# Kernel tuning notes

Hardware: AMD Instinct MI355X
Metric: run time of the kernel (lower is better)

Reference implementation:

```python
import jax, jax.numpy as jnp
import numpy as np
from jax import lax

B = 128; LEADS = 12; T = 1000; DM = 128; DI = 256; DS = 16; DR = 8; DC = 4; NB = 4; L = 199; OUT = 256


def _ln(x, g, b):
    m = x.mean(-1, keepdims=True)
    v = ((x - m) ** 2).mean(-1, keepdims=True)
    return (x - m) * lax.rsqrt(v + 1e-5) * g + b


def _ssm_scan(u, delta, A, Bm, Cm, D):
    """Selective scan. u, delta: [B,L,DI]; Bm, Cm: [B,L,DS]; A: [DI,DS]; D: [DI]."""
    def step(h, inp):
        d_t, B_t, C_t, u_t = inp  # [B,DI],[B,DS],[B,DS],[B,DI]
        dA = jnp.exp(d_t[:, :, None] * A[None])            # [B,DI,DS]
        h = dA * h + (d_t * u_t)[:, :, None] * B_t[:, None, :]
        y = jnp.einsum('bds,bs->bd', h, C_t)
        return h, y
    h0 = jnp.zeros((u.shape[0], A.shape[0], A.shape[1]), u.dtype)
    xs = (jnp.moveaxis(delta, 1, 0), jnp.moveaxis(Bm, 1, 0),
          jnp.moveaxis(Cm, 1, 0), jnp.moveaxis(u, 1, 0))
    _, ys = lax.scan(step, h0, xs)
    return jnp.moveaxis(ys, 0, 1) + u * D[None, None, :]


def setup_inputs() -> dict:
    key = jax.random.key(0)
    ks = jax.random.split(key, 16)
    n = lambda k, shp, s: jax.random.normal(k, shp, jnp.float32) * s
    inp = {}
    inp['x'] = jax.random.normal(ks[0], (B, LEADS, T), jnp.float32)
    inp['pe_w'] = n(ks[1], (DM, LEADS, 10), 0.1)
    inp['pe_b'] = jnp.zeros((DM,), jnp.float32)
    inp['gn_g'] = jnp.ones((DM,), jnp.float32)
    inp['gn_b'] = jnp.zeros((DM,), jnp.float32)
    inp['pos'] = n(ks[2], (1, L, DM), 0.02)
    inp['ln1_g'] = jnp.ones((NB, DM), jnp.float32)
    inp['ln1_b'] = jnp.zeros((NB, DM), jnp.float32)
    inp['in_w'] = n(ks[3], (NB, 2 * DI, DM), 0.05)
    inp['conv_w'] = n(ks[4], (NB, DI, DC), 0.2)
    inp['conv_b'] = jnp.zeros((NB, DI), jnp.float32)
    inp['xproj_w'] = n(ks[5], (NB, DR + 2 * DS, DI), 0.05)
    inp['dtproj_w'] = n(ks[6], (NB, DI, DR), 0.2)
    inp['dtproj_b'] = jnp.full((NB, DI), -4.6, jnp.float32)  # softplus(-4.6) ~= 0.01
    inp['A_log'] = jnp.tile(jnp.log(jnp.arange(1, DS + 1, dtype=jnp.float32))[None, None, :], (NB, DI, 1))
    inp['Dp'] = jnp.ones((NB, DI), jnp.float32)
    inp['outw'] = n(ks[7], (NB, DM, DI), 0.05)
    inp['ln2_g'] = jnp.ones((NB, DM), jnp.float32)
    inp['ln2_b'] = jnp.zeros((NB, DM), jnp.float32)
    inp['ffn_w1'] = n(ks[8], (NB, 4 * DM, DM), 0.05)
    inp['ffn_b1'] = jnp.zeros((NB, 4 * DM), jnp.float32)
    inp['ffn_w2'] = n(ks[9], (NB, DM, 4 * DM), 0.05)
    inp['ffn_b2'] = jnp.zeros((NB, DM), jnp.float32)
    inp['lnf_g'] = jnp.ones((DM,), jnp.float32)
    inp['lnf_b'] = jnp.zeros((DM,), jnp.float32)
    inp['head_w'] = n(ks[10], (OUT, DM), 0.05)
    inp['head_b'] = jnp.zeros((OUT,), jnp.float32)
    return inp


def reference(x, pe_w, pe_b, gn_g, gn_b, pos, ln1_g, ln1_b, in_w, conv_w, conv_b,
              xproj_w, dtproj_w, dtproj_b, A_log, Dp, outw, ln2_g, ln2_b,
              ffn_w1, ffn_b1, ffn_w2, ffn_b2, lnf_g, lnf_b, head_w, head_b):
    # --- patch embed: Conv1d(12 -> DM, k=10, s=5) + GroupNorm(8) + GELU ---
    h = lax.conv_general_dilated(x, pe_w, (5,), 'VALID',
                                 dimension_numbers=('NCH', 'OIH', 'NCH'))
    h = h + pe_b[None, :, None]                      # [B, DM, L]
    Bb, _, Lc = h.shape
    hg = h.reshape(Bb, 8, DM // 8, Lc)
    m = hg.mean((2, 3), keepdims=True)
    v = ((hg - m) ** 2).mean((2, 3), keepdims=True)
    h = ((hg - m) * lax.rsqrt(v + 1e-5)).reshape(Bb, DM, Lc)
    h = h * gn_g[None, :, None] + gn_b[None, :, None]
    h = jax.nn.gelu(h, approximate=False)
    h = jnp.swapaxes(h, 1, 2) + pos                  # [B, L, DM]

    for i in range(NB):
        # --- Mamba block ---
        u = _ln(h, ln1_g[i], ln1_b[i])
        xz = u @ in_w[i].T                           # [B, L, 2*DI]
        xm, z = jnp.split(xz, 2, axis=-1)
        xc = jnp.swapaxes(xm, 1, 2)                  # [B, DI, L]
        xc = jnp.pad(xc, ((0, 0), (0, 0), (DC - 1, 0)))  # causal pad
        xc = lax.conv_general_dilated(xc, conv_w[i][:, None, :], (1,), 'VALID',
                                      dimension_numbers=('NCH', 'OIH', 'NCH'),
                                      feature_group_count=DI)
        xc = xc + conv_b[i][None, :, None]
        u_ssm = jax.nn.silu(jnp.swapaxes(xc, 1, 2))  # [B, L, DI]
        dbl = u_ssm @ xproj_w[i].T                   # [B, L, DR+2*DS]
        dt, Bm, Cm = dbl[..., :DR], dbl[..., DR:DR + DS], dbl[..., DR + DS:]
        delta = jax.nn.softplus(dt @ dtproj_w[i].T + dtproj_b[i])  # [B, L, DI]
        A = -jnp.exp(A_log[i])                       # [DI, DS]
        y = _ssm_scan(u_ssm, delta, A, Bm, Cm, Dp[i])
        y = y * jax.nn.silu(z)
        h = h + y @ outw[i].T
        # --- FFN block ---
        f = _ln(h, ln2_g[i], ln2_b[i])
        f = jax.nn.gelu(f @ ffn_w1[i].T + ffn_b1[i], approximate=False)
        h = h + f @ ffn_w2[i].T + ffn_b2[i]

    h = _ln(h, lnf_g, lnf_b).mean(axis=1)            # [B, DM]
    return jax.nn.gelu(h @ head_w.T + head_b, approximate=False)  # [B, OUT]
```

## Files before the change

kernel.cpp:

```cpp
#include <hip/hip_runtime.h>
#include <math.h>

#define TOKS (128*199)
#define DM 128
#define DI 256
#define DS 16
#define DR 8
#define NBLK 4
#define LSEQ 199
#define BATCH 128

typedef __attribute__((ext_vector_type(8))) short bf16x8;
typedef __attribute__((ext_vector_type(4))) float f32x4;

__device__ __forceinline__ float gelu_f(float x) {
  return 0.5f * x * (1.0f + erff(x * 0.70710678118654752440f));
}
__device__ __forceinline__ float silu_fast(float x) {
  float e = __expf(-x);
  return x * __builtin_amdgcn_rcpf(1.0f + e);
}
__device__ __forceinline__ unsigned short f2bf(float f) {
  unsigned u = __float_as_uint(f);
  u += 0x7fffu + ((u >> 16) & 1u);
  return (unsigned short)(u >> 16);
}
__device__ __forceinline__ float bf2f(unsigned short h) {
  return __uint_as_float(((unsigned)h) << 16);
}

__global__ __launch_bounds__(256) void cvtw_kernel(const float* __restrict__ src,
                                                   unsigned short* __restrict__ dh,
                                                   unsigned short* __restrict__ dl, int n) {
  int i = blockIdx.x*256 + threadIdx.x;
  if (i < n) {
    float v = src[i];
    unsigned short h = f2bf(v);
    dh[i] = h;
    dl[i] = f2bf(v - bf2f(h));
  }
}
__global__ __launch_bounds__(256) void cvtw_pad_kernel(const float* __restrict__ src,
                                                       unsigned short* __restrict__ dh,
                                                       unsigned short* __restrict__ dl) {
  int i = blockIdx.x*256 + threadIdx.x;
  int blk = i >> 14, rem = i & 16383;
  int r = rem >> 8, c = rem & 255;
  float v = (r < 40) ? src[(size_t)blk*40*256 + r*256 + c] : 0.f;
  unsigned short h = f2bf(v);
  dh[i] = h;
  dl[i] = f2bf(v - bf2f(h));
}

__global__ __launch_bounds__(256) void pe_conv_kernel(
    const float* __restrict__ x, const float* __restrict__ pw,
    const float* __restrict__ pb, float* __restrict__ convo) {
  int b = blockIdx.x, tc = blockIdx.y;
  int t0 = tc * 25;
  int nt = (LSEQ - t0 < 25) ? (LSEQ - t0) : 25;
  __shared__ float sx[12][136];
  int tid = threadIdx.x;
  for (int i = tid; i < 12*136; i += 256) {
    int l = i / 136, k = i - l*136;
    int idx = t0*5 + k;
    sx[l][k] = (idx < 1000) ? x[(size_t)b*12000 + l*1000 + idx] : 0.f;
  }
  __syncthreads();
  for (int o = tid; o < DM*nt; o += 256) {
    int m = o / nt, tt = o - m*nt;
    const float* wr = pw + m*120;
    float acc = pb[m];
#pragma unroll
    for (int l = 0; l < 12; ++l) {
#pragma unroll
      for (int k = 0; k < 10; ++k)
        acc += sx[l][tt*5 + k] * wr[l*10 + k];
    }
    convo[((size_t)b*DM + m)*LSEQ + t0 + tt] = acc;
  }
}

__global__ void gn_kernel(const float* __restrict__ conv, const float* __restrict__ gg,
                          const float* __restrict__ gb, const float* __restrict__ pos,
                          float* __restrict__ h) {
  int b = blockIdx.x >> 3, grp = blockIdx.x & 7;
  const float* cb = conv + ((size_t)b*DM + grp*16)*LSEQ;
  int tid = threadIdx.x;
  float s = 0.f, s2 = 0.f;
  for (int i = tid; i < 16*LSEQ; i += 256) { float v = cb[i]; s += v; s2 += v*v; }
#pragma unroll
  for (int m = 1; m < 64; m <<= 1) { s += __shfl_xor(s, m); s2 += __shfl_xor(s2, m); }
  __shared__ float red[8];
  int lane = tid & 63, wid = tid >> 6;
  if (lane == 0) { red[wid] = s; red[4+wid] = s2; }
  __syncthreads();
  float S  = red[0]+red[1]+red[2]+red[3];
  float S2 = red[4]+red[5]+red[6]+red[7];
  const float inv = 1.0f/(16.0f*LSEQ);
  float mean = S*inv;
  float var  = S2*inv - mean*mean;
  float rstd = rsqrtf(var + 1e-5f);
  for (int i = tid; i < 16*LSEQ; i += 256) {
    int mloc = i / LSEQ; int t = i - mloc*LSEQ;
    int m = grp*16 + mloc;
    float v = (cb[i] - mean)*rstd*gg[m] + gb[m];
    v = gelu_f(v);
    h[((size_t)b*LSEQ + t)*DM + m] = v + pos[t*DM + m];
  }
}

__global__ void ln_kernel(const float* __restrict__ x, const float* __restrict__ g,
                          const float* __restrict__ bb,
                          unsigned short* __restrict__ oh, unsigned short* __restrict__ ol) {
  int tok = blockIdx.x*4 + (threadIdx.x >> 6);
  int lane = threadIdx.x & 63;
  const float* xr = x + (size_t)tok*DM;
  float v0 = xr[lane], v1 = xr[lane+64];
  float s = v0+v1, s2 = v0*v0+v1*v1;
#pragma unroll
  for (int m=1;m<64;m<<=1){ s += __shfl_xor(s,m); s2 += __shfl_xor(s2,m); }
  float mean = s*(1.f/DM);
  float var  = s2*(1.f/DM) - mean*mean;
  float rs = rsqrtf(var+1e-5f);
  float y0 = (v0-mean)*rs*g[lane]+bb[lane];
  float y1 = (v1-mean)*rs*g[lane+64]+bb[lane+64];
  size_t o0 = (size_t)tok*DM + lane;
  unsigned short h0 = f2bf(y0), h1 = f2bf(y1);
  oh[o0]    = h0; ol[o0]    = f2bf(y0 - bf2f(h0));
  oh[o0+64] = h1; ol[o0+64] = f2bf(y1 - bf2f(h1));
}

template<int MODE, int BIAS>
__global__ __launch_bounds__(256) void gemm_bf2(
    const unsigned short* __restrict__ Ah, const unsigned short* __restrict__ Al,
    const unsigned short* __restrict__ Wh, const unsigned short* __restrict__ Wl,
    const float* __restrict__ bias,
    float* __restrict__ Cf, unsigned short* __restrict__ Ch, unsigned short* __restrict__ Cl,
    float* __restrict__ Cf2, int N, int K) {
  __shared__ unsigned short lds[2][12288];
  const int tid = threadIdx.x;
  const int w = tid >> 6, l = tid & 63;
  const int fr = l & 15, fq = l >> 4;
  const int frsw = (fr >> 1) & 3;
  const int crow = l >> 2;
  const int ksl = (l & 3) ^ ((l >> 3) & 3);
  const size_t bm0 = (size_t)blockIdx.x * 128;
  const size_t bn0 = (size_t)blockIdx.y * 64;

  const unsigned short* gAh0 = Ah + (bm0 + (size_t)(w*16 + crow))*K + ksl*8;
  const unsigned short* gAh1 = Ah + (bm0 + (size_t)((w+4)*16 + crow))*K + ksl*8;
  const unsigned short* gAl0 = Al + (bm0 + (size_t)(w*16 + crow))*K + ksl*8;
  const unsigned short* gAl1 = Al + (bm0 + (size_t)((w+4)*16 + crow))*K + ksl*8;
  const unsigned short* gWh0 = Wh + (bn0 + (size_t)(w*16 + crow))*K + ksl*8;
  const unsigned short* gWl0 = Wl + (bn0 + (size_t)(w*16 + crow))*K + ksl*8;

  f32x4 acc[2][4];
#pragma unroll
  for (int mi=0;mi<2;++mi)
#pragma unroll
    for (int ns=0;ns<4;++ns) acc[mi][ns] = (f32x4){0.f,0.f,0.f,0.f};

#define STAGE(BUF, KO) do { \
    unsigned short* bb_ = lds[BUF]; \
    __builtin_amdgcn_global_load_lds(gAh0 + (KO), &bb_[w*512],          16, 0, 0); \
    __builtin_amdgcn_global_load_lds(gAh1 + (KO), &bb_[(w+4)*512],      16, 0, 0); \
    __builtin_amdgcn_global_load_lds(gAl0 + (KO), &bb_[4096 + w*512],   16, 0, 0); \
    __builtin_amdgcn_global_load_lds(gAl1 + (KO), &bb_[4096 + (w+4)*512], 16, 0, 0); \
    __builtin_amdgcn_global_load_lds(gWh0 + (KO), &bb_[8192 + w*512],   16, 0, 0); \
    __builtin_amdgcn_global_load_lds(gWl0 + (KO), &bb_[10240 + w*512],  16, 0, 0); \
  } while (0)

  int cur = 0;
  STAGE(0, 0);
  for (int k0 = 0; k0 < K; k0 += 32) {
    __syncthreads();
    if (k0 + 32 < K) STAGE(cur ^ 1, k0 + 32);
    const unsigned short* b = lds[cur];
    bf16x8 whf[4], wlf[4];
#pragma unroll
    for (int ns=0;ns<4;++ns) {
      whf[ns] = *(const bf16x8*)&b[ 8192 + (ns*16 + fr)*32 + ((fq^frsw)*8)];
      wlf[ns] = *(const bf16x8*)&b[10240 + (ns*16 + fr)*32 + ((fq^frsw)*8)];
    }
#pragma unroll
    for (int mi=0;mi<2;++mi) {
      bf16x8 ah = *(const bf16x8*)&b[       (w*32 + mi*16 + fr)*32 + ((fq^frsw)*8)];
      bf16x8 al = *(const bf16x8*)&b[4096 + (w*32 + mi*16 + fr)*32 + ((fq^frsw)*8)];
#pragma unroll
      for (int ns=0;ns<4;++ns) {
        acc[mi][ns] = __builtin_amdgcn_mfma_f32_16x16x32_bf16(ah, whf[ns], acc[mi][ns], 0, 0, 0);
        acc[mi][ns] = __builtin_amdgcn_mfma_f32_16x16x32_bf16(al, whf[ns], acc[mi][ns], 0, 0, 0);
        acc[mi][ns] = __builtin_amdgcn_mfma_f32_16x16x32_bf16(ah, wlf[ns], acc[mi][ns], 0, 0, 0);
      }
    }
    cur ^= 1;
  }
#undef STAGE

  const int row0 = (int)bm0 + w*32;
#pragma unroll
  for (int mi=0;mi<2;++mi) {
#pragma unroll
    for (int ns=0;ns<4;++ns) {
      int col = (int)bn0 + ns*16 + fr;
      float bv = BIAS ? bias[col] : 0.f;
#pragma unroll
      for (int v=0;v<4;++v) {
        float val = acc[mi][ns][v] + bv;
        size_t row = (size_t)(row0 + mi*16 + fq*4 + v);
        if (MODE == 0) {
          Cf[row*N + col] = val;
        } else if (MODE == 1) {
          Cf[row*N + col] += val;
        } else if (MODE == 2) {
          val = gelu_f(val);
          unsigned short hh = f2bf(val);
          Ch[row*N + col] = hh;
          Cl[row*N + col] = f2bf(val - bf2f(hh));
        } else {
          if (col < 256) Cf[row*256 + col] = val;
          else           Cf2[row*256 + (col-256)] = val;
        }
      }
    }
  }
}

__global__ void dwconv_kernel(const float* __restrict__ X, const float* __restrict__ w,
                              const float* __restrict__ bias, float* __restrict__ uss,
                              unsigned short* __restrict__ ussh, unsigned short* __restrict__ ussl) {
  int tok = blockIdx.x;
  int d = threadIdx.x;
  int t = tok % LSEQ;
  float4 wv = *(const float4*)(w + d*4);
  float acc = bias[d];
  const float* xp = X + (size_t)tok*DI + d;
  if (t >= 3) acc += xp[-3*DI]*wv.x;
  if (t >= 2) acc += xp[-2*DI]*wv.y;
  if (t >= 1) acc += xp[-1*DI]*wv.z;
  acc += xp[0]*wv.w;
  float sv = silu_fast(acc);
  size_t o = (size_t)tok*DI + d;
  uss[o] = sv;
  unsigned short hh = f2bf(sv);
  ussh[o] = hh;
  ussl[o] = f2bf(sv - bf2f(hh));
}

__global__ __launch_bounds__(256) void dtproj_kernel(
    const float* __restrict__ dbl, const float* __restrict__ dtw,
    const float* __restrict__ dtb, float* __restrict__ dlt) {
  int tok0 = blockIdx.x * 8;
  int d = threadIdx.x;
  __shared__ float sdt[8][DR];
  if (d < 64) sdt[d >> 3][d & 7] = dbl[(size_t)(tok0 + (d >> 3))*64 + (d & 7)];
  float wreg[DR];
#pragma unroll
  for (int rr = 0; rr < DR; ++rr) wreg[rr] = dtw[d*DR + rr];
  float b0 = dtb[d];
  __syncthreads();
#pragma unroll
  for (int tt = 0; tt < 8; ++tt) {
    float acc = b0;
#pragma unroll
    for (int rr = 0; rr < DR; ++rr) acc += sdt[tt][rr]*wreg[rr];
    acc = (acc > 20.f) ? acc : log1pf(__expf(acc));
    dlt[(size_t)(tok0 + tt)*DI + d] = acc;
  }
}

__global__ __launch_bounds__(256) void scan_kernel(
    const float* __restrict__ uss, const float* __restrict__ dlt,
    const float* __restrict__ dbl,
    const float* __restrict__ A_log, const float* __restrict__ Dp,
    const float* __restrict__ Z,
    unsigned short* __restrict__ yh, unsigned short* __restrict__ yl) {
  int bg = blockIdx.x;
  int b = bg >> 4, dg = bg & 15;
  int tid = threadIdx.x;
  int s = tid & 15, dloc = tid >> 4;
  int d = dg*16 + dloc;
  float As = -__expf(A_log[d*DS + s]);
  float Dd = Dp[d];
  float h = 0.f;
  size_t tokbase = (size_t)b*LSEQ;
  const float* pdt = dlt + tokbase*DI + d;
  const float* pu  = uss + tokbase*DI + d;
  const float* pz  = Z   + tokbase*DI + d;
  const float* pB  = dbl + tokbase*64 + 8  + s;
  const float* pC  = dbl + tokbase*64 + 24 + s;
  size_t ooff = tokbase*DI + d;
  float dt_c = *pdt, u_c = *pu, z_c = *pz, B_c = *pB, C_c = *pC;
  for (int t = 0; t < LSEQ; ++t) {
    float dt = dt_c, u = u_c, z = z_c, Bv = B_c, Cv = C_c;
    if (t + 1 < LSEQ) {
      pdt += DI; pu += DI; pz += DI; pB += 64; pC += 64;
      dt_c = *pdt; u_c = *pu; z_c = *pz; B_c = *pB; C_c = *pC;
    }
    float dA = __expf(dt*As);
    h = fmaf(dA, h, dt*u*Bv);
    float p = h*Cv;
    p += __shfl_xor(p, 1);
    p += __shfl_xor(p, 2);
    p += __shfl_xor(p, 4);
    p += __shfl_xor(p, 8);
    if (s == 0) {
      float yv = fmaf(u, Dd, p) * silu_fast(z);
      unsigned short hh = f2bf(yv);
      yh[ooff] = hh;
      yl[ooff] = f2bf(yv - bf2f(hh));
    }
    ooff += DI;
  }
}

__global__ void final_kernel(const float* __restrict__ h, const float* __restrict__ g,
                             const float* __restrict__ bta, const float* __restrict__ hw,
                             const float* __restrict__ hb, float* __restrict__ out) {
  int b = blockIdx.x;
  int tid = threadIdx.x, lane = tid & 63, wid = tid >> 6;
  float s0 = 0.f, s1 = 0.f;
  for (int t = wid; t < LSEQ; t += 4) {
    const float* hr = h + ((size_t)b*LSEQ + t)*DM;
    float v0 = hr[lane], v1 = hr[lane+64];
    float ss = v0+v1, ss2 = v0*v0+v1*v1;
#pragma unroll
    for (int m=1;m<64;m<<=1){ ss += __shfl_xor(ss,m); ss2 += __shfl_xor(ss2,m); }
    float mean = ss*(1.f/DM);
    float var  = ss2*(1.f/DM)-mean*mean;
    float rs = rsqrtf(var+1e-5f);
    s0 += (v0-mean)*rs*g[lane]+bta[lane];
    s1 += (v1-mean)*rs*g[lane+64]+bta[lane+64];
  }
  __shared__ float sm[4][128];
  sm[wid][lane] = s0; sm[wid][lane+64] = s1;
  __syncthreads();
  __shared__ float mv[128];
  if (tid < 128) mv[tid] = (sm[0][tid]+sm[1][tid]+sm[2][tid]+sm[3][tid]) * (1.f/199.f);
  __syncthreads();
  int j = tid;
  const float* wr = hw + (size_t)j*DM;
  float acc = hb[j];
#pragma unroll 4
  for (int k=0;k<DM;k++) acc += mv[k]*wr[k];
  out[(size_t)b*256 + j] = gelu_f(acc);
}

extern "C" void kernel_launch(void* const* d_in, const int* in_sizes, int n_in,
                              void* d_out, int out_size, void* d_ws, size_t ws_size,
                              hipStream_t stream) {
  const float* x       = (const float*)d_in[0];
  const float* pe_w    = (const float*)d_in[1];
  const float* pe_b    = (const float*)d_in[2];
  const float* gn_g    = (const float*)d_in[3];
  const float* gn_b    = (const float*)d_in[4];
  const float* pos     = (const float*)d_in[5];
  const float* ln1_g   = (const float*)d_in[6];
  const float* ln1_b   = (const float*)d_in[7];
  const float* in_w    = (const float*)d_in[8];
  const float* conv_w  = (const float*)d_in[9];
  const float* conv_b  = (const float*)d_in[10];
  const float* xproj_w = (const float*)d_in[11];
  const float* dtproj_w= (const float*)d_in[12];
  const float* dtproj_b= (const float*)d_in[13];
  const float* A_log   = (const float*)d_in[14];
  const float* Dp      = (const float*)d_in[15];
  const float* outw    = (const float*)d_in[16];
  const float* ln2_g   = (const float*)d_in[17];
  const float* ln2_b   = (const float*)d_in[18];
  const float* ffn_w1  = (const float*)d_in[19];
  const float* ffn_b1  = (const float*)d_in[20];
  const float* ffn_w2  = (const float*)d_in[21];
  const float* ffn_b2  = (const float*)d_in[22];
  const float* lnf_g   = (const float*)d_in[23];
  const float* lnf_b   = (const float*)d_in[24];
  const float* head_w  = (const float*)d_in[25];
  const float* head_b  = (const float*)d_in[26];
  float* out = (float*)d_out;

  float* ws  = (float*)d_ws;
  float* h    = ws;
  float* X    = h   + (size_t)TOKS*DM;
  float* Z    = X   + (size_t)TOKS*DI;
  float* uss  = Z   + (size_t)TOKS*DI;
  float* dlt  = uss + (size_t)TOKS*DI;
  float* dbl  = dlt + (size_t)TOKS*DI;
  unsigned short* uh   = (unsigned short*)(dbl + (size_t)TOKS*64);
  unsigned short* ul   = uh   + (size_t)TOKS*DM;
  unsigned short* ussh = ul   + (size_t)TOKS*DM;
  unsigned short* ussl = ussh + (size_t)TOKS*DI;
  unsigned short* wb   = ussl + (size_t)TOKS*DI;
  unsigned short* inwh = wb;
  unsigned short* inwl = inwh + 262144;
  unsigned short* xpwh = inwl + 262144;
  unsigned short* xpwl = xpwh + 65536;
  unsigned short* outwh= xpwl + 65536;
  unsigned short* outwl= outwh + 131072;
  unsigned short* w1h  = outwl + 131072;
  unsigned short* w1l  = w1h + 262144;
  unsigned short* w2h  = w1l + 262144;
  unsigned short* w2l  = w2h + 262144;
  unsigned short* yh   = (unsigned short*)X;
  unsigned short* yl   = yh + (size_t)TOKS*DI;
  unsigned short* f1h  = (unsigned short*)uss;
  unsigned short* f1l  = f1h + (size_t)TOKS*512;

  cvtw_kernel<<<1024, 256, 0, stream>>>(in_w,   inwh, inwl, 262144);
  cvtw_pad_kernel<<<256, 256, 0, stream>>>(xproj_w, xpwh, xpwl);
  cvtw_kernel<<<512, 256, 0, stream>>>(outw,   outwh, outwl, 131072);
  cvtw_kernel<<<1024, 256, 0, stream>>>(ffn_w1, w1h, w1l, 262144);
  cvtw_kernel<<<1024, 256, 0, stream>>>(ffn_w2, w2h, w2l, 262144);

  pe_conv_kernel<<<dim3(BATCH, 8), 256, 0, stream>>>(x, pe_w, pe_b, X);
  gn_kernel<<<BATCH*8, 256, 0, stream>>>(X, gn_g, gn_b, pos, h);

  for (int i = 0; i < NBLK; ++i) {
    ln_kernel<<<TOKS/4, 256, 0, stream>>>(h, ln1_g + i*DM, ln1_b + i*DM, uh, ul);
    gemm_bf2<3,0><<<dim3(TOKS/128, 8), 256, 0, stream>>>(
        uh, ul, inwh + (size_t)i*65536, inwl + (size_t)i*65536,
        nullptr, X, nullptr, nullptr, Z, 512, DM);
    dwconv_kernel<<<TOKS, 256, 0, stream>>>(X, conv_w + i*DI*4, conv_b + i*DI,
                                            uss, ussh, ussl);
    gemm_bf2<0,0><<<dim3(TOKS/128, 1), 256, 0, stream>>>(
        ussh, ussl, xpwh + (size_t)i*16384, xpwl + (size_t)i*16384,
        nullptr, dbl, nullptr, nullptr, nullptr, 64, DI);
    dtproj_kernel<<<TOKS/8, 256, 0, stream>>>(
        dbl, dtproj_w + (size_t)i*DI*DR, dtproj_b + i*DI, dlt);
    scan_kernel<<<BATCH*16, 256, 0, stream>>>(
        uss, dlt, dbl, A_log + (size_t)i*DI*DS, Dp + i*DI, Z, yh, yl);
    gemm_bf2<1,0><<<dim3(TOKS/128, 2), 256, 0, stream>>>(
        yh, yl, outwh + (size_t)i*32768, outwl + (size_t)i*32768,
        nullptr, h, nullptr, nullptr, nullptr, DM, DI);
    ln_kernel<<<TOKS/4, 256, 0, stream>>>(h, ln2_g + i*DM, ln2_b + i*DM, uh, ul);
    gemm_bf2<2,1><<<dim3(TOKS/128, 8), 256, 0, stream>>>(
        uh, ul, w1h + (size_t)i*65536, w1l + (size_t)i*65536,
        ffn_b1 + i*512, nullptr, f1h, f1l, nullptr, 512, DM);
    gemm_bf2<1,1><<<dim3(TOKS/128, 2), 256, 0, stream>>>(
        f1h, f1l, w2h + (size_t)i*65536, w2l + (size_t)i*65536,
        ffn_b2 + i*DM, h, nullptr, nullptr, nullptr, DM, 512);
  }

  final_kernel<<<BATCH, 256, 0, stream>>>(h, lnf_g, lnf_b, head_w, head_b, out);
}
```

Before: 1.408 ms.

## Retile split-bf16 GEMMs to 2x2 warp grid and fuse SiLU gate into in-proj

```diff
diff --git a/kernel.cpp b/kernel.cpp
--- a/kernel.cpp
+++ b/kernel.cpp
@@ -130,44 +130,49 @@
   oh[o0+64] = h1; ol[o0+64] = f2bf(y1 - bf2f(h1));
 }
 
-template<int MODE, int BIAS>
-__global__ __launch_bounds__(256) void gemm_bf2(
+template<int NSUB, int MODE, int BIAS>
+__global__ __launch_bounds__(256) void gemm_bf3(
     const unsigned short* __restrict__ Ah, const unsigned short* __restrict__ Al,
     const unsigned short* __restrict__ Wh, const unsigned short* __restrict__ Wl,
     const float* __restrict__ bias,
     float* __restrict__ Cf, unsigned short* __restrict__ Ch, unsigned short* __restrict__ Cl,
     float* __restrict__ Cf2, int N, int K) {
-  __shared__ unsigned short lds[2][12288];
+  constexpr int BN   = NSUB*32;
+  constexpr int SZ   = 8192 + NSUB*2048;
+  constexpr int WHOF = 8192;
+  constexpr int WLOF = 8192 + NSUB*1024;
+  __shared__ unsigned short lds[2][SZ];
   const int tid = threadIdx.x;
   const int w = tid >> 6, l = tid & 63;
+  const int wm = w >> 1, wn = w & 1;
   const int fr = l & 15, fq = l >> 4;
-  const int frsw = (fr >> 1) & 3;
-  const int crow = l >> 2;
-  const int ksl = (l & 3) ^ ((l >> 3) & 3);
-  const size_t bm0 = (size_t)blockIdx.x * 128;
-  const size_t bn0 = (size_t)blockIdx.y * 64;
-
-  const unsigned short* gAh0 = Ah + (bm0 + (size_t)(w*16 + crow))*K + ksl*8;
-  const unsigned short* gAh1 = Ah + (bm0 + (size_t)((w+4)*16 + crow))*K + ksl*8;
-  const unsigned short* gAl0 = Al + (bm0 + (size_t)(w*16 + crow))*K + ksl*8;
-  const unsigned short* gAl1 = Al + (bm0 + (size_t)((w+4)*16 + crow))*K + ksl*8;
-  const unsigned short* gWh0 = Wh + (bn0 + (size_t)(w*16 + crow))*K + ksl*8;
-  const unsigned short* gWl0 = Wl + (bn0 + (size_t)(w*16 + crow))*K + ksl*8;
-
-  f32x4 acc[2][4];
-#pragma unroll
-  for (int mi=0;mi<2;++mi)
-#pragma unroll
-    for (int ns=0;ns<4;++ns) acc[mi][ns] = (f32x4){0.f,0.f,0.f,0.f};
+  const size_t bm0 = (size_t)blockIdx.y * 128;
+  const size_t bn0 = (size_t)blockIdx.x * BN;
+  const size_t lane_off = (size_t)(l >> 2)*K + (size_t)(((l & 3) ^ ((l >> 3) & 3)) * 8);
+  const unsigned short* gAh = Ah + bm0*K + lane_off + (size_t)w*16*K;
+  const unsigned short* gAl = Al + bm0*K + lane_off + (size_t)w*16*K;
+  const unsigned short* gWh = Wh + bn0*K + lane_off + (size_t)w*16*K;
+  const unsigned short* gWl = Wl + bn0*K + lane_off + (size_t)w*16*K;
+  const size_t c4 = (size_t)4*16*K;
+
+  f32x4 acc[4][NSUB];
+#pragma unroll
+  for (int m=0;m<4;++m)
+#pragma unroll
+    for (int n=0;n<NSUB;++n) acc[m][n] = (f32x4){0.f,0.f,0.f,0.f};
 
 #define STAGE(BUF, KO) do { \
     unsigned short* bb_ = lds[BUF]; \
-    __builtin_amdgcn_global_load_lds(gAh0 + (KO), &bb_[w*512],          16, 0, 0); \
-    __builtin_amdgcn_global_load_lds(gAh1 + (KO), &bb_[(w+4)*512],      16, 0, 0); \
-    __builtin_amdgcn_global_load_lds(gAl0 + (KO), &bb_[4096 + w*512],   16, 0, 0); \
-    __builtin_amdgcn_global_load_lds(gAl1 + (KO), &bb_[4096 + (w+4)*512], 16, 0, 0); \
-    __builtin_amdgcn_global_load_lds(gWh0 + (KO), &bb_[8192 + w*512],   16, 0, 0); \
-    __builtin_amdgcn_global_load_lds(gWl0 + (KO), &bb_[10240 + w*512],  16, 0, 0); \
+    __builtin_amdgcn_global_load_lds(gAh + (KO),      &bb_[w*512],              16, 0, 0); \
+    __builtin_amdgcn_global_load_lds(gAh + c4 + (KO), &bb_[(w+4)*512],          16, 0, 0); \
+    __builtin_amdgcn_global_load_lds(gAl + (KO),      &bb_[4096 + w*512],       16, 0, 0); \
+    __builtin_amdgcn_global_load_lds(gAl + c4 + (KO), &bb_[4096 + (w+4)*512],   16, 0, 0); \
+    __builtin_amdgcn_global_load_lds(gWh + (KO),      &bb_[WHOF + w*512],       16, 0, 0); \
+    __builtin_amdgcn_global_load_lds(gWl + (KO),      &bb_[WLOF + w*512],       16, 0, 0); \
+    if (NSUB == 4) { \
+      __builtin_amdgcn_global_load_lds(gWh + c4 + (KO), &bb_[WHOF + (w+4)*512], 16, 0, 0); \
+      __builtin_amdgcn_global_load_lds(gWl + c4 + (KO), &bb_[WLOF + (w+4)*512], 16, 0, 0); \
+    } \
   } while (0)
 
   int cur = 0;
@@ -176,38 +181,41 @@
     __syncthreads();
     if (k0 + 32 < K) STAGE(cur ^ 1, k0 + 32);
     const unsigned short* b = lds[cur];
-    bf16x8 whf[4], wlf[4];
-#pragma unroll
-    for (int ns=0;ns<4;++ns) {
-      whf[ns] = *(const bf16x8*)&b[ 8192 + (ns*16 + fr)*32 + ((fq^frsw)*8)];
-      wlf[ns] = *(const bf16x8*)&b[10240 + (ns*16 + fr)*32 + ((fq^frsw)*8)];
+    bf16x8 whf[NSUB], wlf[NSUB];
+#pragma unroll
+    for (int n=0;n<NSUB;++n) {
+      int row = wn*(NSUB*16) + n*16 + fr;
+      int off = row*32 + ((fq ^ ((row>>1)&3))*8);
+      whf[n] = *(const bf16x8*)&b[WHOF + off];
+      wlf[n] = *(const bf16x8*)&b[WLOF + off];
     }
 #pragma unroll
-    for (int mi=0;mi<2;++mi) {
-      bf16x8 ah = *(const bf16x8*)&b[       (w*32 + mi*16 + fr)*32 + ((fq^frsw)*8)];
-      bf16x8 al = *(const bf16x8*)&b[4096 + (w*32 + mi*16 + fr)*32 + ((fq^frsw)*8)];
-#pragma unroll
-      for (int ns=0;ns<4;++ns) {
-        acc[mi][ns] = __builtin_amdgcn_mfma_f32_16x16x32_bf16(ah, whf[ns], acc[mi][ns], 0, 0, 0);
-        acc[mi][ns] = __builtin_amdgcn_mfma_f32_16x16x32_bf16(al, whf[ns], acc[mi][ns], 0, 0, 0);
-        acc[mi][ns] = __builtin_amdgcn_mfma_f32_16x16x32_bf16(ah, wlf[ns], acc[mi][ns], 0, 0, 0);
+    for (int m=0;m<4;++m) {
+      int row = wm*64 + m*16 + fr;
+      int off = row*32 + ((fq ^ ((row>>1)&3))*8);
+      bf16x8 ah = *(const bf16x8*)&b[off];
+      bf16x8 al = *(const bf16x8*)&b[4096 + off];
+#pragma unroll
+      for (int n=0;n<NSUB;++n) {
+        acc[m][n] = __builtin_amdgcn_mfma_f32_16x16x32_bf16(ah, whf[n], acc[m][n], 0, 0, 0);
+        acc[m][n] = __builtin_amdgcn_mfma_f32_16x16x32_bf16(al, whf[n], acc[m][n], 0, 0, 0);
+        acc[m][n] = __builtin_amdgcn_mfma_f32_16x16x32_bf16(ah, wlf[n], acc[m][n], 0, 0, 0);
       }
     }
     cur ^= 1;
   }
 #undef STAGE
 
-  const int row0 = (int)bm0 + w*32;
-#pragma unroll
-  for (int mi=0;mi<2;++mi) {
-#pragma unroll
-    for (int ns=0;ns<4;++ns) {
-      int col = (int)bn0 + ns*16 + fr;
+#pragma unroll
+  for (int m=0;m<4;++m) {
+#pragma unroll
+    for (int n=0;n<NSUB;++n) {
+      int col = (int)bn0 + wn*(NSUB*16) + n*16 + fr;
       float bv = BIAS ? bias[col] : 0.f;
 #pragma unroll
       for (int v=0;v<4;++v) {
-        float val = acc[mi][ns][v] + bv;
-        size_t row = (size_t)(row0 + mi*16 + fq*4 + v);
+        float val = acc[m][n][v] + bv;
+        size_t row = bm0 + wm*64 + m*16 + fq*4 + v;
         if (MODE == 0) {
           Cf[row*N + col] = val;
         } else if (MODE == 1) {
@@ -219,7 +227,7 @@
           Cl[row*N + col] = f2bf(val - bf2f(hh));
         } else {
           if (col < 256) Cf[row*256 + col] = val;
-          else           Cf2[row*256 + (col-256)] = val;
+          else           Cf2[row*256 + (col-256)] = silu_fast(val);
         }
       }
     }
@@ -273,7 +281,7 @@
     const float* __restrict__ uss, const float* __restrict__ dlt,
     const float* __restrict__ dbl,
     const float* __restrict__ A_log, const float* __restrict__ Dp,
-    const float* __restrict__ Z,
+    const float* __restrict__ GZ,
     unsigned short* __restrict__ yh, unsigned short* __restrict__ yl) {
   int bg = blockIdx.x;
   int b = bg >> 4, dg = bg & 15;
@@ -286,17 +294,17 @@
   size_t tokbase = (size_t)b*LSEQ;
   const float* pdt = dlt + tokbase*DI + d;
   const float* pu  = uss + tokbase*DI + d;
-  const float* pz  = Z   + tokbase*DI + d;
+  const float* pgz = GZ  + tokbase*DI + d;
   const float* pB  = dbl + tokbase*64 + 8  + s;
-  const float* pC  = dbl + tokbase*64 + 24 + s;
-  size_t ooff = tokbase*DI + d;
-  float dt_c = *pdt, u_c = *pu, z_c = *pz, B_c = *pB, C_c = *pC;
+  const float* pC  = pB + 16;
+  unsigned short* pyh = yh + tokbase*DI + d;
+  unsigned short* pyl = yl + tokbase*DI + d;
+#pragma unroll 4
   for (int t = 0; t < LSEQ; ++t) {
-    float dt = dt_c, u = u_c, z = z_c, Bv = B_c, Cv = C_c;
-    if (t + 1 < LSEQ) {
-      pdt += DI; pu += DI; pz += DI; pB += 64; pC += 64;
-      dt_c = *pdt; u_c = *pu; z_c = *pz; B_c = *pB; C_c = *pC;
-    }
+    float dt = pdt[(size_t)t*DI];
+    float u  = pu [(size_t)t*DI];
+    float Bv = pB [t*64];
+    float Cv = pC [t*64];
     float dA = __expf(dt*As);
     h = fmaf(dA, h, dt*u*Bv);
     float p = h*Cv;
@@ -305,12 +313,12 @@
     p += __shfl_xor(p, 4);
     p += __shfl_xor(p, 8);
     if (s == 0) {
-      float yv = fmaf(u, Dd, p) * silu_fast(z);
+      float gz = pgz[(size_t)t*DI];
+      float yv = fmaf(u, Dd, p) * gz;
       unsigned short hh = f2bf(yv);
-      yh[ooff] = hh;
-      yl[ooff] = f2bf(yv - bf2f(hh));
+      pyh[(size_t)t*DI] = hh;
+      pyl[(size_t)t*DI] = f2bf(yv - bf2f(hh));
     }
-    ooff += DI;
   }
 }
 
@@ -416,26 +424,26 @@
 
   for (int i = 0; i < NBLK; ++i) {
     ln_kernel<<<TOKS/4, 256, 0, stream>>>(h, ln1_g + i*DM, ln1_b + i*DM, uh, ul);
-    gemm_bf2<3,0><<<dim3(TOKS/128, 8), 256, 0, stream>>>(
+    gemm_bf3<4,3,0><<<dim3(4, 199), 256, 0, stream>>>(
         uh, ul, inwh + (size_t)i*65536, inwl + (size_t)i*65536,
         nullptr, X, nullptr, nullptr, Z, 512, DM);
     dwconv_kernel<<<TOKS, 256, 0, stream>>>(X, conv_w + i*DI*4, conv_b + i*DI,
                                             uss, ussh, ussl);
-    gemm_bf2<0,0><<<dim3(TOKS/128, 1), 256, 0, stream>>>(
+    gemm_bf3<2,0,0><<<dim3(1, 199), 256, 0, stream>>>(
         ussh, ussl, xpwh + (size_t)i*16384, xpwl + (size_t)i*16384,
         nullptr, dbl, nullptr, nullptr, nullptr, 64, DI);
     dtproj_kernel<<<TOKS/8, 256, 0, stream>>>(
         dbl, dtproj_w + (size_t)i*DI*DR, dtproj_b + i*DI, dlt);
     scan_kernel<<<BATCH*16, 256, 0, stream>>>(
         uss, dlt, dbl, A_log + (size_t)i*DI*DS, Dp + i*DI, Z, yh, yl);
-    gemm_bf2<1,0><<<dim3(TOKS/128, 2), 256, 0, stream>>>(
+    gemm_bf3<4,1,0><<<dim3(1, 199), 256, 0, stream>>>(
         yh, yl, outwh + (size_t)i*32768, outwl + (size_t)i*32768,
         nullptr, h, nullptr, nullptr, nullptr, DM, DI);
     ln_kernel<<<TOKS/4, 256, 0, stream>>>(h, ln2_g + i*DM, ln2_b + i*DM, uh, ul);
-    gemm_bf2<2,1><<<dim3(TOKS/128, 8), 256, 0, stream>>>(
+    gemm_bf3<4,2,1><<<dim3(4, 199), 256, 0, stream>>>(
         uh, ul, w1h + (size_t)i*65536, w1l + (size_t)i*65536,
         ffn_b1 + i*512, nullptr, f1h, f1l, nullptr, 512, DM);
-    gemm_bf2<1,1><<<dim3(TOKS/128, 2), 256, 0, stream>>>(
+    gemm_bf3<4,1,1><<<dim3(1, 199), 256, 0, stream>>>(
         f1h, f1l, w2h + (size_t)i*65536, w2l + (size_t)i*65536,
         ffn_b2 + i*DM, h, nullptr, nullptr, nullptr, DM, 512);
   }
```

After: 1.639 ms. +16.5%, slower.
